# Kernel optimization log

Measured on AMD Instinct MI355X. Metric: run time of the kernel, lower is better.

Reference implementation:

```python
import jax, jax.numpy as jnp
import numpy as np

B, L, D, H = 2, 2048, 1024, 16
HD = D // H


def setup_inputs() -> dict:
    key = jax.random.key(0)
    ks = jax.random.split(key, 12)
    s = 1.0 / np.sqrt(D)
    inp = {
        "q": jax.random.normal(ks[0], (B, L, D), jnp.float32),
        "k": jax.random.normal(ks[1], (B, L, D), jnp.float32),
        "v": jax.random.normal(ks[2], (B, L, D), jnp.float32),
        "mask": jnp.zeros((B, L), dtype=bool),  # True = masked out
        "Wq": jax.random.normal(ks[3], (D, D), jnp.float32) * s,
        "bq": jnp.zeros((D,), jnp.float32),
        "Wk": jax.random.normal(ks[4], (D, D), jnp.float32) * s,
        "bk": jnp.zeros((D,), jnp.float32),
        "Wv": jax.random.normal(ks[5], (D, D), jnp.float32) * s,
        "bv": jnp.zeros((D,), jnp.float32),
        "Wo": jax.random.normal(ks[6], (D, D), jnp.float32) * s,
        "bo": jnp.zeros((D,), jnp.float32),
    }
    return inp


def reference(q, k, v, mask, Wq, bq, Wk, bk, Wv, bv, Wo, bo):
    # linear projections (torch Linear: x @ W.T + b), split into heads: [B,H,L,HD]
    def proj(x, W, b):
        y = jnp.einsum('bld,ed->ble', x, W) + b
        return y.reshape(x.shape[0], x.shape[1], H, HD).transpose(0, 2, 1, 3)

    Q = proj(q, Wq, bq)
    K = proj(k, Wk, bk)
    V = proj(v, Wv, bv)

    scale = 1.0 / np.sqrt(HD).astype(np.float32)
    scores = jnp.einsum('bhqd,bhkd->bhqk', Q, K) * scale  # [B,H,Lq,Lk]
    # mask [B,Lk] -> broadcast over heads and query positions
    scores = jnp.where(mask[:, None, None, :], -jnp.inf, scores)
    attn = jax.nn.softmax(scores, axis=-1)
    out = jnp.einsum('bhqk,bhkd->bhqd', attn, V)  # [B,H,Lq,HD]
    out = out.transpose(0, 2, 1, 3).reshape(q.shape[0], q.shape[1], D)
    return jnp.einsum('bld,ed->ble', out, Wo) + bo
```

## Files before the change

### kernel.cpp

```cpp
#include <hip/hip_runtime.h>

#define LSEQ 2048
#define DMODEL 1024
#define NHEAD 16
#define HDIM 64

typedef __attribute__((ext_vector_type(8))) short bf16x8;
typedef __attribute__((ext_vector_type(4))) float f32x4;
typedef __attribute__((ext_vector_type(16))) float f32x16;
typedef unsigned int u32;
typedef unsigned short u16;

static __device__ __forceinline__ u16 f2bf(float x) {
    return (u16)((__builtin_bit_cast(u32, x) + 0x8000u) >> 16);
}

static __device__ __forceinline__ u32 f2bf_pk(float hi, float lo) {
    u32 a = __builtin_bit_cast(u32, hi) + 0x8000u;
    u32 b = __builtin_bit_cast(u32, lo) + 0x8000u;
#if __has_builtin(__builtin_amdgcn_perm)
    return __builtin_amdgcn_perm(a, b, 0x07060302u);
#else
    return (a & 0xFFFF0000u) | (b >> 16);
#endif
}

static __device__ __forceinline__ float fast_exp2(float x) {
#if __has_builtin(__builtin_amdgcn_exp2f)
    return __builtin_amdgcn_exp2f(x);
#else
    return __expf(x * 0.6931471805599453f);
#endif
}

static __device__ __forceinline__ void gll16(const void* g, void* l) {
    __builtin_amdgcn_global_load_lds(
        (const __attribute__((address_space(1))) u32*)g,
        (__attribute__((address_space(3))) u32*)l, 16, 0, 0);
}

__global__ __launch_bounds__(256) void conv_all(
    const float* __restrict__ q, const float* __restrict__ k, const float* __restrict__ v,
    const float* __restrict__ w0, const float* __restrict__ w1,
    const float* __restrict__ w2, const float* __restrict__ w3,
    u16* __restrict__ Qf, u16* __restrict__ Kf, u16* __restrict__ Vf,
    u16* __restrict__ o0, u16* __restrict__ o1, u16* __restrict__ o2,
    u16* __restrict__ o3) {
    const int z = blockIdx.y;
    const float* s; u16* d;
    if (z == 0)      { s = q;  d = Qf; }
    else if (z == 1) { s = k;  d = Kf; }
    else if (z == 2) { s = v;  d = Vf; }
    else if (z == 3) { s = w0; d = o0; }
    else if (z == 4) { s = w1; d = o1; }
    else if (z == 5) { s = w2; d = o2; }
    else             { s = w3; d = o3; }
    if (z >= 3 && blockIdx.x >= 1024) return;
    const int i = (blockIdx.x * 256 + threadIdx.x) * 4;
    float4 x = *(const float4*)(s + i);
    uint2 r;
    r.x = f2bf_pk(x.y, x.x);
    r.y = f2bf_pk(x.w, x.z);
    *(uint2*)(d + i) = r;
}

template <int OUT_MODE>
__device__ __forceinline__ void mfma_gemm(const u16* __restrict__ Xb,
                                          const u16* __restrict__ Wb,
                                          const float* __restrict__ bias,
                                          void* __restrict__ Yv, float scale) {
    __shared__ alignas(16) u16 As[128 * 32];
    __shared__ alignas(16) u16 Bs[128 * 32];

    const int tid = threadIdx.x;
    const int wave = tid >> 6, lane = tid & 63;
    const int l16 = lane & 15, quad = lane >> 4;
    const int wm = (wave >> 1) * 64, wn = (wave & 1) * 64;
    const int m0 = blockIdx.x * 128, n0 = blockIdx.y * 128;

    f32x4 acc[4][4];
    #pragma unroll
    for (int i = 0; i < 4; ++i)
        #pragma unroll
        for (int j = 0; j < 4; ++j)
            #pragma unroll
            for (int r = 0; r < 4; ++r) acc[i][j][r] = 0.0f;

    for (int k0 = 0; k0 < DMODEL; k0 += 32) {
        __syncthreads();
        gll16(Xb + (size_t)(m0 + (tid >> 2)) * DMODEL + k0 + (tid & 3) * 8,
              As + tid * 8);
        gll16(Xb + (size_t)(m0 + 64 + (tid >> 2)) * DMODEL + k0 + (tid & 3) * 8,
              As + 2048 + tid * 8);
        gll16(Wb + (size_t)(n0 + (tid >> 2)) * DMODEL + k0 + (tid & 3) * 8,
              Bs + tid * 8);
        gll16(Wb + (size_t)(n0 + 64 + (tid >> 2)) * DMODEL + k0 + (tid & 3) * 8,
              Bs + 2048 + tid * 8);
        __syncthreads();

        bf16x8 af[4], bf[4];
        #pragma unroll
        for (int mb = 0; mb < 4; ++mb)
            af[mb] = *(const bf16x8*)(As + (wm + mb * 16 + l16) * 32 + quad * 8);
        #pragma unroll
        for (int nb = 0; nb < 4; ++nb)
            bf[nb] = *(const bf16x8*)(Bs + (wn + nb * 16 + l16) * 32 + quad * 8);
        #pragma unroll
        for (int mb = 0; mb < 4; ++mb)
            #pragma unroll
            for (int nb = 0; nb < 4; ++nb)
                acc[mb][nb] = __builtin_amdgcn_mfma_f32_16x16x32_bf16(
                    af[mb], bf[nb], acc[mb][nb], 0, 0, 0);
    }

    #pragma unroll
    for (int nb = 0; nb < 4; ++nb) {
        const int n = n0 + wn + nb * 16 + l16;
        const float bn = bias[n];
        #pragma unroll
        for (int mb = 0; mb < 4; ++mb) {
            const int mb0 = m0 + wm + mb * 16 + quad * 4;
            if (OUT_MODE == 2) {
                u16* Y = (u16*)Yv;
                uint2 rr;
                rr.x = f2bf_pk((acc[mb][nb][1] + bn) * scale, (acc[mb][nb][0] + bn) * scale);
                rr.y = f2bf_pk((acc[mb][nb][3] + bn) * scale, (acc[mb][nb][2] + bn) * scale);
                const int bb = mb0 >> 11, l = mb0 & 2047;
                const int h = n >> 6, hd = n & 63;
                *(uint2*)(Y + ((size_t)((bb * NHEAD + h) * HDIM) + hd) * LSEQ + l) = rr;
            } else {
                #pragma unroll
                for (int r = 0; r < 4; ++r) {
                    const int m = mb0 + r;
                    const float val = (acc[mb][nb][r] + bn) * scale;
                    if (OUT_MODE == 0) {
                        u16* Y = (u16*)Yv;
                        const int bb = m >> 11, l = m & 2047;
                        const int h = n >> 6, hd = n & 63;
                        Y[(((size_t)(bb * NHEAD + h) * LSEQ + l) * HDIM) + hd] = f2bf(val);
                    } else {
                        float* Y = (float*)Yv;
                        Y[(size_t)m * DMODEL + n] = val;
                    }
                }
            }
        }
    }
}

#define QSCALE (0.125f * 1.4426950408889634f)

__global__ __launch_bounds__(256) void qkv_gemm(
    const u16* __restrict__ Qf, const u16* __restrict__ Kf, const u16* __restrict__ Vf,
    const u16* __restrict__ Wqb, const u16* __restrict__ Wkb, const u16* __restrict__ Wvb,
    const float* __restrict__ bq, const float* __restrict__ bk, const float* __restrict__ bv,
    u16* __restrict__ Qp, u16* __restrict__ Kp, u16* __restrict__ Vtp) {
    if (blockIdx.z == 0)      mfma_gemm<0>(Qf, Wqb, bq, (void*)Qp, QSCALE);
    else if (blockIdx.z == 1) mfma_gemm<0>(Kf, Wkb, bk, (void*)Kp, 1.0f);
    else                      mfma_gemm<2>(Vf, Wvb, bv, (void*)Vtp, 1.0f);
}

__global__ __launch_bounds__(256) void out_gemm(
    const u16* __restrict__ AOb, const u16* __restrict__ Wob,
    const float* __restrict__ bo, float* __restrict__ out) {
    mfma_gemm<1>(AOb, Wob, bo, (void*)out, 1.0f);
}

#define KT 128

__global__ __launch_bounds__(256, 2) void attn_mfma(
    const u16* __restrict__ Qp, const u16* __restrict__ Kp,
    const u16* __restrict__ Vtp, const unsigned char* __restrict__ mask,
    u16* __restrict__ AOb) {
    __shared__ alignas(16) u16 smem[32768];

    const int tid = threadIdx.x;
    const int wave = tid >> 6;
    const int lane = tid & 63;
    const int l32 = lane & 31;
    const int half = lane >> 5;
    const int bh = blockIdx.x;
    const int b = bh >> 4;
    const int h = bh & 15;
    const int q0 = blockIdx.y * 128;
    const int qw = q0 + wave * 32;

    const u16* Qg = Qp + ((size_t)bh * LSEQ + qw) * HDIM;
    const u16* Kg = Kp + (size_t)bh * LSEQ * HDIM;
    const u16* Vtg = Vtp + (size_t)bh * HDIM * LSEQ;
    const unsigned char* mg = mask + (size_t)b * LSEQ;

    bf16x8 qf[4];
    #pragma unroll
    for (int dc = 0; dc < 4; ++dc)
        qf[dc] = *(const bf16x8*)(Qg + (size_t)l32 * HDIM + dc * 16 + half * 8);

    f32x16 o0 = {}, o1 = {};
    float l_l = 0.0f;

    auto stage = [&](int ktile, int buf) {
        const int k0 = ktile * KT;
        u16* Kb = smem + buf * 8192;
        u16* Vb = smem + 16384 + buf * 8192;
        #pragma unroll
        for (int j = 0; j < 4; ++j) {
            const int cid = j * 256 + tid;
            const int key = cid >> 3, pc = cid & 7, c = pc ^ (key & 7);
            gll16(Kg + (size_t)(k0 + key) * HDIM + c * 8, Kb + cid * 8);
        }
        #pragma unroll
        for (int j = 0; j < 4; ++j) {
            const int cid = j * 256 + tid;
            const int d = cid >> 4, pc = cid & 15, c = pc ^ (d & 15);
            gll16(Vtg + (size_t)d * LSEQ + k0 + c * 8, Vb + cid * 8);
        }
    };

    stage(0, 0);

    for (int kt = 0; kt < LSEQ / KT; ++kt) {
        const int cur = kt & 1;
        const u16* Kb = smem + cur * 8192;
        const u16* Vb = smem + 16384 + cur * 8192;
        const int k0 = kt * KT;
        const int mb0 = mg[k0 + lane];
        const int mb1 = mg[k0 + 64 + lane];

        __syncthreads();
        if (kt + 1 < LSEQ / KT) stage(kt + 1, cur ^ 1);

        f32x16 st[4];
        #pragma unroll
        for (int kb = 0; kb < 4; ++kb) st[kb] = (f32x16)(0.0f);
        #pragma unroll
        for (int dc = 0; dc < 4; ++dc)
            #pragma unroll
            for (int kb = 0; kb < 4; ++kb) {
                const int key = kb * 32 + l32;
                const int phys = (dc * 2 + half) ^ (key & 7);
                bf16x8 kf = *(const bf16x8*)(Kb + key * 64 + phys * 8);
                st[kb] = __builtin_amdgcn_mfma_f32_32x32x16_bf16(kf, qf[dc], st[kb], 0, 0, 0);
            }

        const unsigned long long anym = __ballot(mb0 | mb1);
        if (anym) {
            const float b0f = mb0 ? -1e30f : 0.0f;
            const float b1f = mb1 ? -1e30f : 0.0f;
            #pragma unroll
            for (int kb = 0; kb < 4; ++kb)
                #pragma unroll
                for (int r = 0; r < 16; ++r) {
                    const int key = kb * 32 + (r & 3) + 8 * (r >> 2) + 4 * half;
                    const float bv = __shfl((kb < 2) ? b0f : b1f, key & 63, 64);
                    st[kb][r] += bv;
                }
        }

        u32 pk[4][8];
        #pragma unroll
        for (int kb = 0; kb < 4; ++kb)
            #pragma unroll
            for (int w = 0; w < 8; ++w) {
                const float plo = fast_exp2(st[kb][2 * w]);
                const float phi = fast_exp2(st[kb][2 * w + 1]);
                l_l += plo + phi;
                pk[kb][w] = f2bf_pk(phi, plo);
            }

        #pragma unroll
        for (int c = 0; c < 8; ++c) {
            const int kb = c >> 1, wb = 4 * (c & 1);
            const u32 ta = half ? pk[kb][wb] : pk[kb][wb + 2];
            const u32 tb = half ? pk[kb][wb + 1] : pk[kb][wb + 3];
            const u32 xa = __shfl_xor((int)ta, 32, 64);
            const u32 xb = __shfl_xor((int)tb, 32, 64);
            u32 w4[4];
            w4[0] = half ? xa : pk[kb][wb];
            w4[1] = half ? xb : pk[kb][wb + 1];
            w4[2] = half ? pk[kb][wb + 2] : xa;
            w4[3] = half ? pk[kb][wb + 3] : xb;
            bf16x8 pb = __builtin_bit_cast(bf16x8, *(uint4*)w4);
            {
                const int d = l32;
                const int phys = (c * 2 + half) ^ (d & 15);
                bf16x8 va = *(const bf16x8*)(Vb + d * 128 + phys * 8);
                o0 = __builtin_amdgcn_mfma_f32_32x32x16_bf16(va, pb, o0, 0, 0, 0);
            }
            {
                const int d = 32 + l32;
                const int phys = (c * 2 + half) ^ (d & 15);
                bf16x8 va = *(const bf16x8*)(Vb + d * 128 + phys * 8);
                o1 = __builtin_amdgcn_mfma_f32_32x32x16_bf16(va, pb, o1, 0, 0, 0);
            }
        }
    }

    const float l_tot = l_l + __shfl_xor(l_l, 32, 64);
    const float inv = 1.0f / l_tot;
    __syncthreads();
    u16* T = smem;
    #pragma unroll
    for (int nb = 0; nb < 2; ++nb)
        #pragma unroll
        for (int rp = 0; rp < 8; ++rp) {
            const int r = rp * 2;
            const int d = nb * 32 + (r & 3) + 8 * (r >> 2) + 4 * half;
            const float vlo = (nb ? o1[r] : o0[r]) * inv;
            const float vhi = (nb ? o1[r + 1] : o0[r + 1]) * inv;
            *(u32*)(T + (wave * 32 + l32) * 72 + d) = f2bf_pk(vhi, vlo);
        }
    __syncthreads();
    #pragma unroll
    for (int i = 0; i < 4; ++i) {
        const int cid = i * 256 + tid;
        const int row = cid >> 3, ch = cid & 7;
        bf16x8 val = *(const bf16x8*)(T + row * 72 + ch * 8);
        *(bf16x8*)(AOb + ((size_t)(b * LSEQ + q0 + row) * DMODEL) + h * HDIM + ch * 8) = val;
    }
}

extern "C" void kernel_launch(void* const* d_in, const int* in_sizes, int n_in,
                              void* d_out, int out_size, void* d_ws, size_t ws_size,
                              hipStream_t stream) {
    (void)in_sizes; (void)n_in; (void)out_size; (void)ws_size;
    const float* q  = (const float*)d_in[0];
    const float* k  = (const float*)d_in[1];
    const float* v  = (const float*)d_in[2];
    const unsigned char* mask = (const unsigned char*)d_in[3];
    const float* Wq = (const float*)d_in[4];
    const float* bq = (const float*)d_in[5];
    const float* Wk = (const float*)d_in[6];
    const float* bk = (const float*)d_in[7];
    const float* Wv = (const float*)d_in[8];
    const float* bv = (const float*)d_in[9];
    const float* Wo = (const float*)d_in[10];
    const float* bo = (const float*)d_in[11];
    float* out = (float*)d_out;

    u16* ws16 = (u16*)d_ws;
    const size_t M4 = (size_t)4 * 1024 * 1024;
    const size_t M1 = (size_t)1024 * 1024;
    u16* Qf  = ws16;
    u16* Kf  = ws16 + M4;
    u16* Vf  = ws16 + 2 * M4;
    u16* Qp  = ws16 + 3 * M4;
    u16* Kp  = ws16 + 4 * M4;
    u16* Vtp = ws16 + 5 * M4;
    u16* AOb = ws16 + 6 * M4;
    u16* Wqb = ws16 + 7 * M4;
    u16* Wkb = ws16 + 7 * M4 + M1;
    u16* Wvb = ws16 + 7 * M4 + 2 * M1;
    u16* Wob = ws16 + 7 * M4 + 3 * M1;

    conv_all<<<dim3(4096, 7), 256, 0, stream>>>(q, k, v, Wq, Wk, Wv, Wo,
                                                Qf, Kf, Vf, Wqb, Wkb, Wvb, Wob);
    qkv_gemm<<<dim3(32, 8, 3), 256, 0, stream>>>(Qf, Kf, Vf, Wqb, Wkb, Wvb,
                                                 bq, bk, bv, Qp, Kp, Vtp);
    attn_mfma<<<dim3(32, 16), 256, 0, stream>>>(Qp, Kp, Vtp, mask, AOb);
    out_gemm<<<dim3(32, 8), 256, 0, stream>>>(AOb, Wob, bo, out);
}
```

Baseline: 235.8 us.

## Double-buffer GEMM LDS tiles and use smaller tiles for output projection

Templates the MFMA GEMM on tile sizes and switches from a load-sync-compute-sync loop to a two-buffer LDS scheme. The next K-slice is prefetched while the current one is multiplied, leaving one barrier per iteration instead of two. The output projection now uses 64x64 tiles with four times as many blocks to fill the CUs better, and launch bounds hint occupancy. The cost is double the LDS per block and, for the 64x64 tiles, less operand reuse per block.

```diff
diff --git a/kernel.cpp b/kernel.cpp
--- a/kernel.cpp
+++ b/kernel.cpp
@@ -64,61 +64,77 @@
     *(uint2*)(d + i) = r;
 }
 
-template <int OUT_MODE>
+template <int TM, int TN, int OUT_MODE>
 __device__ __forceinline__ void mfma_gemm(const u16* __restrict__ Xb,
                                           const u16* __restrict__ Wb,
                                           const float* __restrict__ bias,
                                           void* __restrict__ Yv, float scale) {
-    __shared__ alignas(16) u16 As[128 * 32];
-    __shared__ alignas(16) u16 Bs[128 * 32];
+    constexpr int MB = TM / 32;
+    constexpr int NB = TN / 32;
+    __shared__ alignas(16) u16 As[2 * TM * 32];
+    __shared__ alignas(16) u16 Bs[2 * TN * 32];
 
     const int tid = threadIdx.x;
     const int wave = tid >> 6, lane = tid & 63;
     const int l16 = lane & 15, quad = lane >> 4;
-    const int wm = (wave >> 1) * 64, wn = (wave & 1) * 64;
-    const int m0 = blockIdx.x * 128, n0 = blockIdx.y * 128;
-
-    f32x4 acc[4][4];
-    #pragma unroll
-    for (int i = 0; i < 4; ++i)
-        #pragma unroll
-        for (int j = 0; j < 4; ++j)
+    const int wm = (wave >> 1) * (TM / 2), wn = (wave & 1) * (TN / 2);
+    const int m0 = blockIdx.x * TM, n0 = blockIdx.y * TN;
+
+    f32x4 acc[MB][NB];
+    #pragma unroll
+    for (int i = 0; i < MB; ++i)
+        #pragma unroll
+        for (int j = 0; j < NB; ++j)
             #pragma unroll
             for (int r = 0; r < 4; ++r) acc[i][j][r] = 0.0f;
 
-    for (int k0 = 0; k0 < DMODEL; k0 += 32) {
+    auto stage = [&](int k0, int buf) {
+        u16* Ab = As + buf * TM * 32;
+        u16* Bb = Bs + buf * TN * 32;
+        #pragma unroll
+        for (int j = 0; j < TM / 64; ++j) {
+            const int cid = j * 256 + tid;
+            const int row = cid >> 2, c = cid & 3;
+            gll16(Xb + (size_t)(m0 + row) * DMODEL + k0 + c * 8, Ab + cid * 8);
+        }
+        #pragma unroll
+        for (int j = 0; j < TN / 64; ++j) {
+            const int cid = j * 256 + tid;
+            const int row = cid >> 2, c = cid & 3;
+            gll16(Wb + (size_t)(n0 + row) * DMODEL + k0 + c * 8, Bb + cid * 8);
+        }
+    };
+
+    stage(0, 0);
+
+    for (int i = 0; i < DMODEL / 32; ++i) {
+        const int cur = i & 1;
         __syncthreads();
-        gll16(Xb + (size_t)(m0 + (tid >> 2)) * DMODEL + k0 + (tid & 3) * 8,
-              As + tid * 8);
-        gll16(Xb + (size_t)(m0 + 64 + (tid >> 2)) * DMODEL + k0 + (tid & 3) * 8,
-              As + 2048 + tid * 8);
-        gll16(Wb + (size_t)(n0 + (tid >> 2)) * DMODEL + k0 + (tid & 3) * 8,
-              Bs + tid * 8);
-        gll16(Wb + (size_t)(n0 + 64 + (tid >> 2)) * DMODEL + k0 + (tid & 3) * 8,
-              Bs + 2048 + tid * 8);
-        __syncthreads();
-
-        bf16x8 af[4], bf[4];
-        #pragma unroll
-        for (int mb = 0; mb < 4; ++mb)
-            af[mb] = *(const bf16x8*)(As + (wm + mb * 16 + l16) * 32 + quad * 8);
-        #pragma unroll
-        for (int nb = 0; nb < 4; ++nb)
-            bf[nb] = *(const bf16x8*)(Bs + (wn + nb * 16 + l16) * 32 + quad * 8);
-        #pragma unroll
-        for (int mb = 0; mb < 4; ++mb)
-            #pragma unroll
-            for (int nb = 0; nb < 4; ++nb)
+        if (i + 1 < DMODEL / 32) stage((i + 1) * 32, cur ^ 1);
+
+        const u16* Ab = As + cur * TM * 32;
+        const u16* Bb = Bs + cur * TN * 32;
+        bf16x8 af[MB], bf[NB];
+        #pragma unroll
+        for (int mb = 0; mb < MB; ++mb)
+            af[mb] = *(const bf16x8*)(Ab + (wm + mb * 16 + l16) * 32 + quad * 8);
+        #pragma unroll
+        for (int nb = 0; nb < NB; ++nb)
+            bf[nb] = *(const bf16x8*)(Bb + (wn + nb * 16 + l16) * 32 + quad * 8);
+        #pragma unroll
+        for (int mb = 0; mb < MB; ++mb)
+            #pragma unroll
+            for (int nb = 0; nb < NB; ++nb)
                 acc[mb][nb] = __builtin_amdgcn_mfma_f32_16x16x32_bf16(
                     af[mb], bf[nb], acc[mb][nb], 0, 0, 0);
     }
 
     #pragma unroll
-    for (int nb = 0; nb < 4; ++nb) {
+    for (int nb = 0; nb < NB; ++nb) {
         const int n = n0 + wn + nb * 16 + l16;
         const float bn = bias[n];
         #pragma unroll
-        for (int mb = 0; mb < 4; ++mb) {
+        for (int mb = 0; mb < MB; ++mb) {
             const int mb0 = m0 + wm + mb * 16 + quad * 4;
             if (OUT_MODE == 2) {
                 u16* Y = (u16*)Yv;
@@ -150,20 +166,20 @@
 
 #define QSCALE (0.125f * 1.4426950408889634f)
 
-__global__ __launch_bounds__(256) void qkv_gemm(
+__global__ __launch_bounds__(256, 3) void qkv_gemm(
     const u16* __restrict__ Qf, const u16* __restrict__ Kf, const u16* __restrict__ Vf,
     const u16* __restrict__ Wqb, const u16* __restrict__ Wkb, const u16* __restrict__ Wvb,
     const float* __restrict__ bq, const float* __restrict__ bk, const float* __restrict__ bv,
     u16* __restrict__ Qp, u16* __restrict__ Kp, u16* __restrict__ Vtp) {
-    if (blockIdx.z == 0)      mfma_gemm<0>(Qf, Wqb, bq, (void*)Qp, QSCALE);
-    else if (blockIdx.z == 1) mfma_gemm<0>(Kf, Wkb, bk, (void*)Kp, 1.0f);
-    else                      mfma_gemm<2>(Vf, Wvb, bv, (void*)Vtp, 1.0f);
-}
-
-__global__ __launch_bounds__(256) void out_gemm(
+    if (blockIdx.z == 0)      mfma_gemm<128, 128, 0>(Qf, Wqb, bq, (void*)Qp, QSCALE);
+    else if (blockIdx.z == 1) mfma_gemm<128, 128, 0>(Kf, Wkb, bk, (void*)Kp, 1.0f);
+    else                      mfma_gemm<128, 128, 2>(Vf, Wvb, bv, (void*)Vtp, 1.0f);
+}
+
+__global__ __launch_bounds__(256, 4) void out_gemm(
     const u16* __restrict__ AOb, const u16* __restrict__ Wob,
     const float* __restrict__ bo, float* __restrict__ out) {
-    mfma_gemm<1>(AOb, Wob, bo, (void*)out, 1.0f);
+    mfma_gemm<64, 64, 1>(AOb, Wob, bo, (void*)out, 1.0f);
 }
 
 #define KT 128
@@ -357,5 +373,5 @@
     qkv_gemm<<<dim3(32, 8, 3), 256, 0, stream>>>(Qf, Kf, Vf, Wqb, Wkb, Wvb,
                                                  bq, bk, bv, Qp, Kp, Vtp);
     attn_mfma<<<dim3(32, 16), 256, 0, stream>>>(Qp, Kp, Vtp, mask, AOb);
-    out_gemm<<<dim3(32, 8), 256, 0, stream>>>(AOb, Wob, bo, out);
-}
+    out_gemm<<<dim3(64, 16), 256, 0, stream>>>(AOb, Wob, bo, out);
+}
```

Measured after the change: 239.2 us. Within noise of the previous version (+1.4%).
